# Kernel tuning notes

Hardware: AMD Instinct MI355X
Metric: run time of the kernel (lower is better)

Reference implementation:

```python
import jax, jax.numpy as jnp
import numpy as np

DIM = 1024
HEADS = 16
DHEAD = 64
MAXLEN = 512
B = 8
N = 256   # sequence (x) length
M = 256   # memory (h) length; M + N <= MAXLEN
INNER = HEADS * DHEAD


def setup_inputs() -> dict:
    key = jax.random.key(0)
    ks = jax.random.split(key, 8)
    w = lambda k, shape: jax.random.normal(k, shape, jnp.float32) * 0.02
    return {
        "x": jax.random.normal(ks[0], (B, N, DIM), jnp.float32),
        "h": jax.random.normal(ks[1], (B, M, DIM), jnp.float32),
        "Wqkv": w(ks[2], (DIM, 3 * INNER)),
        "Wkr": w(ks[3], (DIM, INNER)),
        "R": jax.random.normal(ks[4], (2 * MAXLEN, DIM), jnp.float32),
        "u": jax.random.normal(ks[5], (DHEAD,), jnp.float32),
        "v": jax.random.normal(ks[6], (DHEAD,), jnp.float32),
        "Wout": w(ks[7], (INNER, DIM)),
        "max_len": MAXLEN,
    }


def reference(x, h, Wqkv, Wkr, R, u, v, Wout, max_len):
    b, n, dim = x.shape
    m = h.shape[1]
    t = m + n
    scale = DHEAD ** -0.5

    cat = jnp.concatenate([h, x], axis=1)                     # [b, t, dim]
    qkv = cat @ Wqkv                                          # [b, t, 3*inner]
    q, k, val = [s.reshape(b, t, HEADS, DHEAD).transpose(0, 2, 1, 3)
                 for s in jnp.split(qkv, 3, axis=-1)]          # [b, h, t, d]

    # shifts[i, j] = (j - i) mod 2L, sliced as in the torch buffer
    ar = jnp.arange(2 * max_len)
    shifts_full = (ar[None, :] - ar[:, None]) % (2 * max_len)
    shifts = shifts_full[:max_len, :max_len][m:m + n, :t]      # [n, t]

    kr = (R @ Wkr)[shifts]                                    # gather: [n, t, inner]
    kr = kr.reshape(n, t, HEADS, DHEAD).transpose(2, 0, 1, 3)  # [h, n, t, d]

    q = q[:, :, m:]                                           # [b, h, n, d]

    term_a = jnp.einsum('bhnd,bhmd->bhnm', q, k)
    term_b = jnp.einsum('bhnd,hnmd->bhnm', q, kr)
    term_c = jnp.einsum('d,bhmd->bhm', u, k)[:, :, None, :]    # broadcast over n
    term_d = jnp.einsum('d,hnmd->hnm', v, kr)[None]            # broadcast over b
    dots = (term_a + term_b + term_c + term_d) * scale         # [b, h, n, t]

    qi = jnp.arange(n)[:, None]
    jm = jnp.arange(m)[None, :]
    js = jnp.arange(n)[None, :]
    mem_mask = jnp.where(qi > jm, -jnp.inf, 0.0)               # [n, m]
    ar_mask = jnp.where(js > qi, -jnp.inf, 0.0)                # [n, n]
    bias = jnp.concatenate([mem_mask, ar_mask], axis=1)[None, None]  # [1,1,n,t]

    attn = jax.nn.softmax(dots + bias, axis=-1)
    out = jnp.einsum('bhnm,bhmd->bhnd', attn, val)             # [b, h, n, d]
    out = out.transpose(0, 2, 1, 3).reshape(b, n, INNER)
    return out @ Wout
```

## Files before the change

kernel.cpp:

```cpp
#include <hip/hip_runtime.h>
#include <hip/hip_bf16.h>
#include <math.h>

typedef unsigned short u16;
typedef short bf16x8 __attribute__((ext_vector_type(8)));
typedef float f32x4 __attribute__((ext_vector_type(4)));

__device__ __forceinline__ u16 f2b(float f) {
    __hip_bfloat16 h = __float2bfloat16(f);
    return *reinterpret_cast<u16*>(&h);
}
__device__ __forceinline__ float b2f(u16 v) {
    __hip_bfloat16 h;
    *reinterpret_cast<u16*>(&h) = v;
    return __bfloat162float(h);
}

__device__ __forceinline__ void gload_lds16(const void* g, void* l) {
    __builtin_amdgcn_global_load_lds(
        (const __attribute__((address_space(1))) void*)g,
        (__attribute__((address_space(3))) void*)l, 16, 0, 0);
}


struct EpiQKV4 {
    u16 *Q, *Kt, *Vt;
    __device__ void operator()(int rowp, int colp, f32x4 vals) const {
        int b = colp >> 9, pos = colp & 511;
        int sec = rowp >> 10, cc = rowp & 1023;
        int head = cc >> 6, d0 = cc & 63;
        if (sec == 0) {
            if (pos < 256) return;
            ushort4 o;
            o.x = f2b(vals[0] * 0.125f); o.y = f2b(vals[1] * 0.125f);
            o.z = f2b(vals[2] * 0.125f); o.w = f2b(vals[3] * 0.125f);
            *(ushort4*)(Q + (long)((head * 8 + b) * 256 + (pos - 256)) * 64 + d0) = o;
        } else if (sec == 1) {
            ushort4 o;
            o.x = f2b(vals[0]); o.y = f2b(vals[1]);
            o.z = f2b(vals[2]); o.w = f2b(vals[3]);
            *(ushort4*)(Kt + (long)((b * 16 + head) * 512 + pos) * 64 + d0) = o;
        } else {
            #pragma unroll
            for (int r = 0; r < 4; ++r)
                Vt[(long)((b * 16 + head) * 64 + d0 + r) * 512 + pos] = f2b(vals[r]);
        }
    }
};

__global__ __launch_bounds__(256) void prep_kernel(const float* __restrict__ x,
                                                   const float* __restrict__ h,
                                                   u16* __restrict__ catBF,
                                                   const float* __restrict__ Wqkv, u16* __restrict__ WqkvT,
                                                   const float* __restrict__ Wkr,  u16* __restrict__ WkrT,
                                                   const float* __restrict__ Wout, u16* __restrict__ WoutT,
                                                   const float* __restrict__ R,   u16* __restrict__ Rg,
                                                   u16* __restrict__ vtGuard) {
    __shared__ float tile[64][65];
    int bid = blockIdx.x, tid = threadIdx.x;
    if (bid == 3520) {
        ((unsigned int*)vtGuard)[tid] = 0u;
        return;
    }
    if (bid >= 3328) {
        int idx = ((bid - 3328) * 256 + tid) * 8;
        int row = idx >> 10, c = idx & 1023;
        int srow = (row < 256) ? 768 + row : 0;
        const float* src = R + (long)srow * 1024 + c;
        float4 f0 = *(const float4*)src;
        float4 f1 = *(const float4*)(src + 4);
        bf16x8 vv;
        vv[0] = (short)f2b(f0.x); vv[1] = (short)f2b(f0.y);
        vv[2] = (short)f2b(f0.z); vv[3] = (short)f2b(f0.w);
        vv[4] = (short)f2b(f1.x); vv[5] = (short)f2b(f1.y);
        vv[6] = (short)f2b(f1.z); vv[7] = (short)f2b(f1.w);
        *(bf16x8*)(Rg + idx) = vv;
        return;
    }
    if (bid < 2048) {
        int idx = (bid * 256 + tid) * 8;
        int c = idx & 1023, r = idx >> 10;
        int b = r >> 9, pos = r & 511;
        const float* src = (pos < 256) ? h + ((long)(b * 256 + pos) * 1024 + c)
                                       : x + ((long)(b * 256 + pos - 256) * 1024 + c);
        float4 f0 = *(const float4*)src;
        float4 f1 = *(const float4*)(src + 4);
        bf16x8 vv;
        vv[0] = (short)f2b(f0.x); vv[1] = (short)f2b(f0.y);
        vv[2] = (short)f2b(f0.z); vv[3] = (short)f2b(f0.w);
        vv[4] = (short)f2b(f1.x); vv[5] = (short)f2b(f1.y);
        vv[6] = (short)f2b(f1.z); vv[7] = (short)f2b(f1.w);
        *(bf16x8*)(catBF + idx) = vv;
        return;
    }
    const float* W; u16* WT; int nb, kb; long ldw;
    int w = bid - 2048;
    if (w < 768) {
        W = Wqkv; WT = WqkvT; ldw = 3072;
        nb = (w % 48) * 64; kb = (w / 48) * 64;
    } else if (w < 1024) {
        int w2 = w - 768;
        W = Wkr; WT = WkrT; ldw = 1024;
        nb = (w2 & 15) * 64; kb = (w2 >> 4) * 64;
    } else {
        int w2 = w - 1024;
        W = Wout; WT = WoutT; ldw = 1024;
        nb = (w2 & 15) * 64; kb = (w2 >> 4) * 64;
    }
    {
        int lr = tid >> 4, lc = (tid & 15) * 4;
        #pragma unroll
        for (int i = 0; i < 4; ++i) {
            float4 v = *(const float4*)&W[(long)(kb + lr + i * 16) * ldw + nb + lc];
            tile[lr + i * 16][lc + 0] = v.x; tile[lr + i * 16][lc + 1] = v.y;
            tile[lr + i * 16][lc + 2] = v.z; tile[lr + i * 16][lc + 3] = v.w;
        }
    }
    __syncthreads();
    {
        int wr = tid >> 2, wc = (tid & 3) * 16;
        #pragma unroll
        for (int k = 0; k < 2; ++k) {
            bf16x8 vv;
            #pragma unroll
            for (int e = 0; e < 8; ++e)
                vv[e] = (short)f2b(tile[wc + k * 8 + e][wr]);
            *(bf16x8*)(WT + (long)(nb + wr) * 1024 + kb + wc + k * 8) = vv;
        }
    }
}

__global__ __launch_bounds__(256, 3) void qkv_rwg_kernel(const u16* __restrict__ A, const u16* __restrict__ B,
                                                         EpiQKV4 eq,
                                                         const u16* __restrict__ Rg, const u16* __restrict__ WkrT,
                                                         u16* __restrict__ RWg) {
    __shared__ alignas(16) char smem[49152];
    int bid0 = blockIdx.x;
    bool isRW = bid0 >= 640;
    int m0, n0;
    const u16 *Ag, *Bg;
    if (isRW) {
        int b2 = bid0 - 640;
        m0 = (b2 >> 3) * 128;
        n0 = (b2 & 7) * 128;
        Ag = Rg; Bg = WkrT;
    } else {
        int xcd = bid0 & 7, s = bid0 >> 3;
        int t0i = s >> 3;
        int w = s & 7;
        if (t0i < 8) {
            int nchunk = xcd >> 1;
            int mrow = (xcd & 1) * 8 + t0i;
            m0 = 1024 + mrow * 128;
            n0 = (nchunk * 8 + w) * 128;
        } else {
            int qidx = xcd * 2 + (t0i - 8);
            int nchunk = qidx >> 3, mrow = qidx & 7;
            m0 = mrow * 128;
            int c = nchunk * 8 + w;
            n0 = (c >> 1) * 512 + 256 + (c & 1) * 128;
        }
        Ag = A; Bg = B;
    }
    int tid = threadIdx.x, wave = tid >> 6, lane = tid & 63;
    int wm = wave >> 1, wn = wave & 1;
    int lrow = lane & 15, lquad = lane >> 4;
    const u16* Ab = Ag + (long)m0 * 1024;
    const u16* Bb = Bg + (long)n0 * 1024;
    f32x4 acc[4][4] = {};

    int scperm = (((tid & 3) - ((tid >> 3) & 3)) & 3) * 8;
    int rsl = ((lquad + (lrow >> 1)) & 3) * 8;

    auto stage = [&](int buf, int k0) {
        u16* Asb = (u16*)smem + buf * 8192;
        u16* Bsb = Asb + 4096;
        int col = k0 + scperm;
        #pragma unroll
        for (int i = 0; i < 2; ++i) {
            int rowb = i * 64 + (tid >> 2);
            gload_lds16(Ab + (long)rowb * 1024 + col, Asb + i * 2048 + tid * 8);
            gload_lds16(Bb + (long)rowb * 1024 + col, Bsb + i * 2048 + tid * 8);
        }
    };
    auto compute = [&](int buf) {
        u16* Asb = (u16*)smem + buf * 8192;
        u16* Bsb = Asb + 4096;
        bf16x8 af[4], bfr[4];
        #pragma unroll
        for (int mt = 0; mt < 4; ++mt)
            af[mt] = *(const bf16x8*)(Asb + (wm * 64 + mt * 16 + lrow) * 32 + rsl);
        #pragma unroll
        for (int nt = 0; nt < 4; ++nt)
            bfr[nt] = *(const bf16x8*)(Bsb + (wn * 64 + nt * 16 + lrow) * 32 + rsl);
        #pragma unroll
        for (int mt = 0; mt < 4; ++mt)
            #pragma unroll
            for (int nt = 0; nt < 4; ++nt)
                acc[mt][nt] = __builtin_amdgcn_mfma_f32_16x16x32_bf16(af[mt], bfr[nt], acc[mt][nt], 0, 0, 0);
    };

    stage(0, 0);
    stage(1, 32);
    int cb = 0, sb = 2;
    for (int t = 0; t < 32; ++t) {
        if (t < 31) {
            asm volatile("s_waitcnt vmcnt(4)" ::: "memory");
        } else {
            asm volatile("s_waitcnt vmcnt(0)" ::: "memory");
        }
        __builtin_amdgcn_sched_barrier(0);
        __builtin_amdgcn_s_barrier();
        __builtin_amdgcn_sched_barrier(0);
        compute(cb);
        __builtin_amdgcn_sched_barrier(0);
        if (t < 30) stage(sb, (t + 2) * 32);
        cb = (cb == 2) ? 0 : cb + 1;
        sb = (sb == 2) ? 0 : sb + 1;
    }

    if (isRW) {
        #pragma unroll
        for (int mt = 0; mt < 4; ++mt)
            #pragma unroll
            for (int nt = 0; nt < 4; ++nt) {
                int rowp = m0 + wm * 64 + mt * 16 + lquad * 4;
                int colp = n0 + wn * 64 + nt * 16 + lrow;
                #pragma unroll
                for (int r = 0; r < 4; ++r)
                    RWg[(long)(rowp + r) * 1024 + colp] = f2b(acc[mt][nt][r]);
            }
    } else {
        #pragma unroll
        for (int mt = 0; mt < 4; ++mt)
            #pragma unroll
            for (int nt = 0; nt < 4; ++nt) {
                int rowp = m0 + wm * 64 + mt * 16 + lquad * 4;
                int colp = n0 + wn * 64 + nt * 16 + lrow;
                eq(rowp, colp, acc[mt][nt]);
            }
    }
}

__global__ __launch_bounds__(256, 4) void outproj_kernel(const u16* __restrict__ A,
                                                         const u16* __restrict__ B,
                                                         float* __restrict__ out) {
    __shared__ alignas(16) char smem[16384];
    int bid = blockIdx.x;
    int n0 = (bid & 15) * 64, m0 = (bid >> 4) * 64;
    int tid = threadIdx.x, wave = tid >> 6, lane = tid & 63;
    int wm = wave >> 1, wn = wave & 1;
    int lrow = lane & 15, lquad = lane >> 4;
    const u16* Ab = A + (long)m0 * 1024;
    const u16* Bb = B + (long)n0 * 1024;
    f32x4 acc[2][2] = {};

    int scperm = (((tid & 3) - ((tid >> 3) & 3)) & 3) * 8;
    int rsl = ((lquad + (lrow >> 1)) & 3) * 8;

    auto stage = [&](int buf, int k0) {
        u16* Asb = (u16*)smem + buf * 4096;
        u16* Bsb = Asb + 2048;
        int row = tid >> 2, col = k0 + scperm;
        gload_lds16(Ab + (long)row * 1024 + col, Asb + tid * 8);
        gload_lds16(Bb + (long)row * 1024 + col, Bsb + tid * 8);
    };
    auto compute = [&](int buf) {
        u16* Asb = (u16*)smem + buf * 4096;
        u16* Bsb = Asb + 2048;
        bf16x8 af[2], bfr[2];
        #pragma unroll
        for (int mt = 0; mt < 2; ++mt)
            af[mt] = *(const bf16x8*)(Asb + (wm * 32 + mt * 16 + lrow) * 32 + rsl);
        #pragma unroll
        for (int nt = 0; nt < 2; ++nt)
            bfr[nt] = *(const bf16x8*)(Bsb + (wn * 32 + nt * 16 + lrow) * 32 + rsl);
        #pragma unroll
        for (int mt = 0; mt < 2; ++mt)
            #pragma unroll
            for (int nt = 0; nt < 2; ++nt)
                acc[mt][nt] = __builtin_amdgcn_mfma_f32_16x16x32_bf16(af[mt], bfr[nt], acc[mt][nt], 0, 0, 0);
    };

    stage(0, 0);
    stage(1, 32);
    for (int t = 0; t < 31; ++t) {
        asm volatile("s_waitcnt vmcnt(2)" ::: "memory");
        __builtin_amdgcn_sched_barrier(0);
        __builtin_amdgcn_s_barrier();
        __builtin_amdgcn_sched_barrier(0);
        compute(t & 1);
        __builtin_amdgcn_sched_barrier(0);
        __builtin_amdgcn_s_barrier();
        __builtin_amdgcn_sched_barrier(0);
        if (t < 30) stage(t & 1, (t + 2) * 32);
    }
    asm volatile("s_waitcnt vmcnt(0)" ::: "memory");
    __builtin_amdgcn_sched_barrier(0);
    __builtin_amdgcn_s_barrier();
    __builtin_amdgcn_sched_barrier(0);
    compute(1);

    #pragma unroll
    for (int mt = 0; mt < 2; ++mt)
        #pragma unroll
        for (int nt = 0; nt < 2; ++nt)
            #pragma unroll
            for (int r = 0; r < 4; ++r)
                out[(long)(m0 + wm * 32 + mt * 16 + lquad * 4 + r) * 1024
                    + n0 + wn * 32 + nt * 16 + lrow] = acc[mt][nt][r];
}

__global__ __launch_bounds__(256, 4) void attn_kernel(const u16* __restrict__ Qs,
                                                      const u16* __restrict__ Kt,
                                                      const u16* __restrict__ VT,
                                                      const u16* __restrict__ RWg,
                                                      const float* __restrict__ uvec,
                                                      const float* __restrict__ vvec,
                                                      u16* __restrict__ attnOut) {
    constexpr int LDSW = 360;
    __shared__ alignas(16) u16 SQ[32 * LDSW];
    __shared__ float red[2][4][32];
    int xcd = blockIdx.x & 7, local = blockIdx.x >> 3;
    int bh = xcd * 16 + (local & 15);
    int it = local >> 4;
    int b = bh >> 4, h = bh & 15;
    int i0 = it * 32;
    int w0 = i0;
    int tid = threadIdx.x, wave = tid >> 6, lane = tid & 63;
    int lrow = lane & 15, lquad = lane >> 4;

    bf16x8 aq[2][2], aqv[2][2];
    #pragma unroll
    for (int iu = 0; iu < 2; ++iu) {
        const u16* qbase = Qs + (long)((h * 8 + b) * 256 + i0 + iu * 16 + lrow) * 64;
        bf16x8 q0 = *(const bf16x8*)(qbase + lquad * 8);
        bf16x8 q1 = *(const bf16x8*)(qbase + 32 + lquad * 8);
        #pragma unroll
        for (int j = 0; j < 8; ++j) {
            float f0 = b2f((u16)q0[j]), f1 = b2f((u16)q1[j]);
            aq[iu][0][j]  = (short)f2b(f0 + 0.125f * uvec[lquad * 8 + j]);
            aq[iu][1][j]  = (short)f2b(f1 + 0.125f * uvec[32 + lquad * 8 + j]);
            aqv[iu][0][j] = (short)f2b(f0 + 0.125f * vvec[lquad * 8 + j]);
            aqv[iu][1][j] = (short)f2b(f1 + 0.125f * vvec[32 + lquad * 8 + j]);
        }
    }

    const u16* rwbase = RWg + (long)(wave * 80) * 1024 + h * 64;
    #pragma unroll
    for (int t = 0; t < 5; ++t) {
        const u16* rp = rwbase + (long)(t * 16 + lrow) * 1024;
        bf16x8 br0 = *(const bf16x8*)(rp + lquad * 8);
        bf16x8 br1 = *(const bf16x8*)(rp + 32 + lquad * 8);
        int sc = wave * 80 + t * 16 + lrow;
        #pragma unroll
        for (int iu = 0; iu < 2; ++iu) {
            f32x4 qa = {0.f, 0.f, 0.f, 0.f};
            qa = __builtin_amdgcn_mfma_f32_16x16x32_bf16(aqv[iu][0], br0, qa, 0, 0, 0);
            qa = __builtin_amdgcn_mfma_f32_16x16x32_bf16(aqv[iu][1], br1, qa, 0, 0, 0);
            #pragma unroll
            for (int r = 0; r < 4; ++r) {
                int rloc = iu * 16 + lquad * 4 + r;
                SQ[rloc * LDSW + sc + rloc] = f2b(qa[r]);
            }
        }
    }

    const u16* kbase = Kt + ((long)bh * 512 + w0 + wave * 80) * 64;
    bf16x8 bk0[5], bk1[5];
    #pragma unroll
    for (int t = 0; t < 5; ++t) {
        const u16* kp = kbase + (long)(t * 16 + lrow) * 64;
        bk0[t] = *(const bf16x8*)(kp + lquad * 8);
        bk1[t] = *(const bf16x8*)(kp + 32 + lquad * 8);
    }
    f32x4 acc[2][5];
    __builtin_amdgcn_s_setprio(1);
    #pragma unroll
    for (int t = 0; t < 5; ++t)
        #pragma unroll
        for (int iu = 0; iu < 2; ++iu) {
            f32x4 a = {0.f, 0.f, 0.f, 0.f};
            a = __builtin_amdgcn_mfma_f32_16x16x32_bf16(aq[iu][0], bk0[t], a, 0, 0, 0);
            a = __builtin_amdgcn_mfma_f32_16x16x32_bf16(aq[iu][1], bk1[t], a, 0, 0, 0);
            acc[iu][t] = a;
        }
    __builtin_amdgcn_s_setprio(0);
    __syncthreads();

    float m4[2][4];
    #pragma unroll
    for (int iu = 0; iu < 2; ++iu)
        #pragma unroll
        for (int r = 0; r < 4; ++r) m4[iu][r] = -1e30f;
    #pragma unroll
    for (int t = 0; t < 5; ++t) {
        int lj = wave * 80 + t * 16 + lrow;
        #pragma unroll
        for (int iu = 0; iu < 2; ++iu)
            #pragma unroll
            for (int r = 0; r < 4; ++r) {
                int rloc = iu * 16 + lquad * 4 + r;
                bool ok = (unsigned)(lj - rloc) <= 256u;
                float val = ok ? acc[iu][t][r] + b2f(SQ[rloc * LDSW + lj]) : -1e30f;
                acc[iu][t][r] = val;
                m4[iu][r] = fmaxf(m4[iu][r], val);
            }
    }
    #pragma unroll
    for (int iu = 0; iu < 2; ++iu)
        #pragma unroll
        for (int r = 0; r < 4; ++r) {
            #pragma unroll
            for (int off = 1; off < 16; off <<= 1)
                m4[iu][r] = fmaxf(m4[iu][r], __shfl_xor(m4[iu][r], off));
            if (lrow == 0) red[0][wave][iu * 16 + lquad * 4 + r] = m4[iu][r];
        }
    __syncthreads();

    float gmax[2][4];
    #pragma unroll
    for (int iu = 0; iu < 2; ++iu)
        #pragma unroll
        for (int r = 0; r < 4; ++r) {
            int row = iu * 16 + lquad * 4 + r;
            gmax[iu][r] = fmaxf(fmaxf(red[0][0][row], red[0][1][row]),
                                fmaxf(red[0][2][row], red[0][3][row]));
        }

    float s4[2][4] = {};
    #pragma unroll
    for (int t = 0; t < 5; ++t) {
        int lj = wave * 80 + t * 16 + lrow;
        #pragma unroll
        for (int iu = 0; iu < 2; ++iu)
            #pragma unroll
            for (int r = 0; r < 4; ++r) {
                float p = __expf(acc[iu][t][r] - gmax[iu][r]);
                s4[iu][r] += p;
                SQ[(iu * 16 + lquad * 4 + r) * LDSW + lj] = f2b(p);
            }
    }
    #pragma unroll
    for (int iu = 0; iu < 2; ++iu)
        #pragma unroll
        for (int r = 0; r < 4; ++r) {
            #pragma unroll
            for (int off = 1; off < 16; off <<= 1)
                s4[iu][r] += __shfl_xor(s4[iu][r], off);
            if (lrow == 0) red[1][wave][iu * 16 + lquad * 4 + r] = s4[iu][r];
        }
    __syncthreads();

    const u16* vbase = VT + ((long)bh * 64 + wave * 16 + lrow) * 512 + w0;
    f32x4 oacc[2] = {};
    bf16x8 vp[10];
    #pragma unroll
    for (int t = 0; t < 10; ++t)
        vp[t] = *(const bf16x8*)(vbase + t * 32 + lquad * 8);
    __builtin_amdgcn_s_setprio(1);
    #pragma unroll
    for (int t = 0; t < 10; ++t)
        #pragma unroll
        for (int iu = 0; iu < 2; ++iu) {
            bf16x8 ap = *(const bf16x8*)(SQ + (iu * 16 + lrow) * LDSW + t * 32 + lquad * 8);
            oacc[iu] = __builtin_amdgcn_mfma_f32_16x16x32_bf16(ap, vp[t], oacc[iu], 0, 0, 0);
        }
    __builtin_amdgcn_s_setprio(0);
    #pragma unroll
    for (int iu = 0; iu < 2; ++iu)
        #pragma unroll
        for (int r = 0; r < 4; ++r) {
            int row = iu * 16 + lquad * 4 + r;
            float inv = 1.0f / (red[1][0][row] + red[1][1][row] + red[1][2][row] + red[1][3][row]);
            attnOut[(long)(b * 256 + i0 + row) * 1024 + h * 64 + wave * 16 + lrow] = f2b(oacc[iu][r] * inv);
        }
}


extern "C" void kernel_launch(void* const* d_in, const int* in_sizes, int n_in,
                              void* d_out, int out_size, void* d_ws, size_t ws_size,
                              hipStream_t stream) {
    (void)in_sizes; (void)n_in; (void)out_size; (void)ws_size;
    const float* x    = (const float*)d_in[0];
    const float* h    = (const float*)d_in[1];
    const float* Wqkv = (const float*)d_in[2];
    const float* Wkr  = (const float*)d_in[3];
    const float* R    = (const float*)d_in[4];
    const float* u    = (const float*)d_in[5];
    const float* v    = (const float*)d_in[6];
    const float* Wout = (const float*)d_in[7];
    float* out = (float*)d_out;

    char* ws = (char*)d_ws;
    size_t off = 0;
    auto alloc = [&](size_t bytes) -> void* {
        void* p = ws + off;
        off = (off + bytes + 255) & ~(size_t)255;
        return p;
    };
    u16* catBF  = (u16*)alloc(4096L * 1024 * 2);
    u16* WqkvT  = (u16*)alloc(3072L * 1024 * 2);
    u16* WkrT   = (u16*)alloc(1024L * 1024 * 2);
    u16* WoutT  = (u16*)alloc(1024L * 1024 * 2);
    u16* Rg     = (u16*)alloc(384L * 1024 * 2);
    u16* RWg    = (u16*)alloc(384L * 1024 * 2);
    u16* Q      = (u16*)alloc(16L * 8 * 256 * 64 * 2);
    u16* Kt     = (u16*)alloc(8L * 16 * 512 * 64 * 2);
    u16* VT     = (u16*)alloc(8L * 16 * 64 * 512 * 2 + 1024);
    u16* attnO  = (u16*)alloc(2048L * 1024 * 2);
    u16* vtGuard = VT + 8L * 16 * 64 * 512;

    prep_kernel<<<3521, 256, 0, stream>>>(x, h, catBF, Wqkv, WqkvT, Wkr, WkrT, Wout, WoutT, R, Rg, vtGuard);
    qkv_rwg_kernel<<<664, 256, 0, stream>>>(WqkvT, catBF, EpiQKV4{Q, Kt, VT}, Rg, WkrT, RWg);
    attn_kernel<<<1024, 256, 0, stream>>>(Q, Kt, VT, RWg, u, v, attnO);
    outproj_kernel<<<512, 256, 0, stream>>>(attnO, WoutT, out);
}
```

Before: 159.9 us.

## Triple-buffer outproj, widen prep conversion per thread, change attn block mapping

The outproj GEMM moves from double to triple LDS buffering, which drops the second barrier per k-step so global loads can overlap compute. The prep kernel has each thread convert 16 floats instead of 8 for the cat and R conversions, cutting the block count. The attn kernel replaces the XCD-aware block-to-(batch,head) mapping with a plain linear mapping. Together these aim to cut barrier stalls and launch overhead, at the cost of more LDS per block and possibly worse L2 locality in attention.

Result: no change. 161.3 us (+0.9%).

```diff
diff --git a/kernel.cpp b/kernel.cpp
--- a/kernel.cpp
+++ b/kernel.cpp
@@ -20,6 +20,15 @@
     __builtin_amdgcn_global_load_lds(
         (const __attribute__((address_space(1))) void*)g,
         (__attribute__((address_space(3))) void*)l, 16, 0, 0);
+}
+
+__device__ __forceinline__ bf16x8 cvt2bf8(float4 f0, float4 f1) {
+    bf16x8 vv;
+    vv[0] = (short)f2b(f0.x); vv[1] = (short)f2b(f0.y);
+    vv[2] = (short)f2b(f0.z); vv[3] = (short)f2b(f0.w);
+    vv[4] = (short)f2b(f1.x); vv[5] = (short)f2b(f1.y);
+    vv[6] = (short)f2b(f1.z); vv[7] = (short)f2b(f1.w);
+    return vv;
 }
 
 
@@ -58,43 +67,31 @@
                                                    u16* __restrict__ vtGuard) {
     __shared__ float tile[64][65];
     int bid = blockIdx.x, tid = threadIdx.x;
-    if (bid == 3520) {
+    if (bid == 2400) {
         ((unsigned int*)vtGuard)[tid] = 0u;
         return;
     }
-    if (bid >= 3328) {
-        int idx = ((bid - 3328) * 256 + tid) * 8;
-        int row = idx >> 10, c = idx & 1023;
-        int srow = (row < 256) ? 768 + row : 0;
-        const float* src = R + (long)srow * 1024 + c;
-        float4 f0 = *(const float4*)src;
-        float4 f1 = *(const float4*)(src + 4);
-        bf16x8 vv;
-        vv[0] = (short)f2b(f0.x); vv[1] = (short)f2b(f0.y);
-        vv[2] = (short)f2b(f0.z); vv[3] = (short)f2b(f0.w);
-        vv[4] = (short)f2b(f1.x); vv[5] = (short)f2b(f1.y);
-        vv[6] = (short)f2b(f1.z); vv[7] = (short)f2b(f1.w);
-        *(bf16x8*)(Rg + idx) = vv;
-        return;
-    }
-    if (bid < 2048) {
-        int idx = (bid * 256 + tid) * 8;
+    if (bid < 1024) {
+        int idx = (bid * 256 + tid) * 16;
         int c = idx & 1023, r = idx >> 10;
         int b = r >> 9, pos = r & 511;
         const float* src = (pos < 256) ? h + ((long)(b * 256 + pos) * 1024 + c)
                                        : x + ((long)(b * 256 + pos - 256) * 1024 + c);
-        float4 f0 = *(const float4*)src;
-        float4 f1 = *(const float4*)(src + 4);
-        bf16x8 vv;
-        vv[0] = (short)f2b(f0.x); vv[1] = (short)f2b(f0.y);
-        vv[2] = (short)f2b(f0.z); vv[3] = (short)f2b(f0.w);
-        vv[4] = (short)f2b(f1.x); vv[5] = (short)f2b(f1.y);
-        vv[6] = (short)f2b(f1.z); vv[7] = (short)f2b(f1.w);
-        *(bf16x8*)(catBF + idx) = vv;
+        *(bf16x8*)(catBF + idx)     = cvt2bf8(*(const float4*)src,       *(const float4*)(src + 4));
+        *(bf16x8*)(catBF + idx + 8) = cvt2bf8(*(const float4*)(src + 8), *(const float4*)(src + 12));
         return;
     }
+    if (bid >= 2304) {
+        int idx = ((bid - 2304) * 256 + tid) * 16;
+        int row = idx >> 10, c = idx & 1023;
+        int srow = (row < 256) ? 768 + row : 0;
+        const float* src = R + (long)srow * 1024 + c;
+        *(bf16x8*)(Rg + idx)     = cvt2bf8(*(const float4*)src,       *(const float4*)(src + 4));
+        *(bf16x8*)(Rg + idx + 8) = cvt2bf8(*(const float4*)(src + 8), *(const float4*)(src + 12));
+        return;
+    }
     const float* W; u16* WT; int nb, kb; long ldw;
-    int w = bid - 2048;
+    int w = bid - 1024;
     if (w < 768) {
         W = Wqkv; WT = WqkvT; ldw = 3072;
         nb = (w % 48) * 64; kb = (w / 48) * 64;
@@ -245,7 +242,7 @@
 __global__ __launch_bounds__(256, 4) void outproj_kernel(const u16* __restrict__ A,
                                                          const u16* __restrict__ B,
                                                          float* __restrict__ out) {
-    __shared__ alignas(16) char smem[16384];
+    __shared__ alignas(16) char smem[24576];
     int bid = blockIdx.x;
     int n0 = (bid & 15) * 64, m0 = (bid >> 4) * 64;
     int tid = threadIdx.x, wave = tid >> 6, lane = tid & 63;
@@ -284,22 +281,22 @@
 
     stage(0, 0);
     stage(1, 32);
-    for (int t = 0; t < 31; ++t) {
-        asm volatile("s_waitcnt vmcnt(2)" ::: "memory");
+    int cb = 0, sb = 2;
+    for (int t = 0; t < 32; ++t) {
+        if (t < 31) {
+            asm volatile("s_waitcnt vmcnt(2)" ::: "memory");
+        } else {
+            asm volatile("s_waitcnt vmcnt(0)" ::: "memory");
+        }
         __builtin_amdgcn_sched_barrier(0);
         __builtin_amdgcn_s_barrier();
         __builtin_amdgcn_sched_barrier(0);
-        compute(t & 1);
+        compute(cb);
         __builtin_amdgcn_sched_barrier(0);
-        __builtin_amdgcn_s_barrier();
-        __builtin_amdgcn_sched_barrier(0);
-        if (t < 30) stage(t & 1, (t + 2) * 32);
-    }
-    asm volatile("s_waitcnt vmcnt(0)" ::: "memory");
-    __builtin_amdgcn_sched_barrier(0);
-    __builtin_amdgcn_s_barrier();
-    __builtin_amdgcn_sched_barrier(0);
-    compute(1);
+        if (t < 30) stage(sb, (t + 2) * 32);
+        cb = (cb == 2) ? 0 : cb + 1;
+        sb = (sb == 2) ? 0 : sb + 1;
+    }
 
     #pragma unroll
     for (int mt = 0; mt < 2; ++mt)
@@ -321,9 +318,8 @@
     constexpr int LDSW = 360;
     __shared__ alignas(16) u16 SQ[32 * LDSW];
     __shared__ float red[2][4][32];
-    int xcd = blockIdx.x & 7, local = blockIdx.x >> 3;
-    int bh = xcd * 16 + (local & 15);
-    int it = local >> 4;
+    int id = blockIdx.x;
+    int bh = id & 127, it = id >> 7;
     int b = bh >> 4, h = bh & 15;
     int i0 = it * 32;
     int w0 = i0;
@@ -511,7 +507,7 @@
     u16* attnO  = (u16*)alloc(2048L * 1024 * 2);
     u16* vtGuard = VT + 8L * 16 * 64 * 512;
 
-    prep_kernel<<<3521, 256, 0, stream>>>(x, h, catBF, Wqkv, WqkvT, Wkr, WkrT, Wout, WoutT, R, Rg, vtGuard);
+    prep_kernel<<<2401, 256, 0, stream>>>(x, h, catBF, Wqkv, WqkvT, Wkr, WkrT, Wout, WoutT, R, Rg, vtGuard);
     qkv_rwg_kernel<<<664, 256, 0, stream>>>(WqkvT, catBF, EpiQKV4{Q, Kt, VT}, Rg, WkrT, RWg);
     attn_kernel<<<1024, 256, 0, stream>>>(Q, Kt, VT, RWg, u, v, attnO);
     outproj_kernel<<<512, 256, 0, stream>>>(attnO, WoutT, out);
```
